# Kernel tuning notes

Hardware: AMD Instinct MI355X
Metric: run time of the kernel (lower is better)

Reference implementation:

```python
import jax, jax.numpy as jnp
import numpy as np

N_NODES = 32768
N_EDGES = 524288
EPS = 1e-5

def _layernorm(h):
    mu = jnp.mean(h, axis=-1, keepdims=True)
    var = jnp.var(h, axis=-1, keepdims=True)
    return (h - mu) / jnp.sqrt(var + EPS)

def _leaky_relu(h):
    return jnp.where(h >= 0, h, 0.01 * h)

def setup_inputs() -> dict:
    key = jax.random.key(0)
    ks = jax.random.split(key, 16)
    F, H, D = 256, 256, 1024
    x = jax.random.normal(ks[0], (N_NODES, F), dtype=jnp.float32)
    src = jax.random.randint(ks[1], (N_EDGES,), 0, N_NODES, dtype=jnp.int32)
    dst = jax.random.randint(ks[2], (N_EDGES,), 0, N_NODES, dtype=jnp.int32)
    dims = [F, H, H, H, D]
    params = {}
    for i in range(4):
        params[f"W{i+1}"] = jax.random.normal(ks[3 + i], (dims[i], dims[i + 1]), dtype=jnp.float32) * (1.0 / np.sqrt(dims[i]))
        params[f"b{i+1}"] = jnp.zeros((dims[i + 1],), dtype=jnp.float32)
    Wm = jax.random.normal(ks[8], (D, D), dtype=jnp.float32) * (1.0 / np.sqrt(D))
    bm = jnp.zeros((D,), dtype=jnp.float32)
    Ws = jax.random.normal(ks[9], (D, D), dtype=jnp.float32) * (1.0 / np.sqrt(D))
    bs = jnp.zeros((D,), dtype=jnp.float32)
    return dict(x=x, src=src, dst=dst, W1=params["W1"], b1=params["b1"], W2=params["W2"], b2=params["b2"], W3=params["W3"], b3=params["b3"], W4=params["W4"], b4=params["b4"], Wm=Wm, bm=bm, Ws=Ws, bs=bs, batch_b=128, nodes_per=256)

def reference(x, src, dst, W1, b1, W2, b2, W3, b3, W4, b4, Wm, bm, Ws, bs, batch_b, nodes_per):
    # DGL GraphConv norm='both': out = D_in^{-1/2} * A @ (D_out^{-1/2} * h) @ W + b
    ones = jnp.ones((src.shape[0],), dtype=x.dtype)
    out_deg = jax.ops.segment_sum(ones, src, num_segments=N_NODES)
    in_deg = jax.ops.segment_sum(ones, dst, num_segments=N_NODES)
    ns = jnp.where(out_deg > 0, jax.lax.rsqrt(out_deg), 1.0)[:, None]
    nd = jnp.where(in_deg > 0, jax.lax.rsqrt(in_deg), 1.0)[:, None]

    def gconv(h, W, b):
        if W.shape[0] <= W.shape[1]:  # aggregate first, then project (in <= out)
            m = (h * ns)[src]
            agg = jax.ops.segment_sum(m, dst, num_segments=N_NODES) * nd
            return agg @ W + b
        else:  # project first
            h = (h * ns) @ W
            agg = jax.ops.segment_sum(h[src], dst, num_segments=N_NODES) * nd
            return agg + b

    h = x
    for (W, b) in [(W1, b1), (W2, b2), (W3, b3), (W4, b4)]:
        h = _layernorm(_leaky_relu(gconv(h, W, b)))
    h = h.reshape(batch_b, nodes_per, -1)  # [B, N_per, D]
    h = jnp.mean(h, axis=1)                # AvePool over nodes
    h = _layernorm(h)
    mean = h @ Wm + bm
    log_std = h @ Ws + bs
    return (mean, log_std)
```

## Files before the change

### kernel.cpp

```cpp
#include <hip/hip_runtime.h>

#define N_NODES 32768
#define N_EDGES 524288

typedef __attribute__((ext_vector_type(8))) short short8;
typedef __attribute__((ext_vector_type(4))) float floatx4;

#define GLOBAL_AS __attribute__((address_space(1)))
#define LDS_AS __attribute__((address_space(3)))

__device__ __forceinline__ unsigned short f2bf(float x) {
    union { float f; unsigned u; } v; v.f = x;
    unsigned r = v.u + 0x7FFF + ((v.u >> 16) & 1);
    return (unsigned short)(r >> 16);
}
__device__ __forceinline__ float bf2f(unsigned short u) {
    union { unsigned u; float f; } v; v.u = ((unsigned)u) << 16;
    return v.f;
}


__global__ __launch_bounds__(256) void k_hist(const int* __restrict__ src,
                                              const int* __restrict__ dst,
                                              unsigned int* __restrict__ histOut32,
                                              unsigned int* __restrict__ histIn32) {
    __shared__ unsigned int hOut[8192];
    __shared__ unsigned int hIn[8192];
    int t = threadIdx.x, b = blockIdx.x;
    for (int i = t; i < 8192; i += 256) { hOut[i] = 0; hIn[i] = 0; }
    __syncthreads();
    int base = b * 4096;
    for (int i = t; i < 4096; i += 256) {
        int s = src[base + i], d = dst[base + i];
        atomicAdd(&hOut[s >> 2], 1u << ((s & 3) * 8));
        atomicAdd(&hIn[d >> 2], 1u << ((d & 3) * 8));
    }
    __syncthreads();
    for (int i = t; i < 8192; i += 256) {
        histOut32[b * 8192 + i] = hOut[i];
        histIn32[b * 8192 + i] = hIn[i];
    }
}

__global__ __launch_bounds__(256) void k_merge(const unsigned int* __restrict__ histOut32,
                                               const unsigned int* __restrict__ histIn32,
                                               unsigned int* __restrict__ pre32,
                                               int* __restrict__ in_deg,
                                               float* __restrict__ ns,
                                               float* __restrict__ nd) {
    int g = blockIdx.x * 256 + threadIdx.x;
    int ri0 = 0, ri1 = 0, ri2 = 0, ri3 = 0;
    for (int b = 0; b < 128; b++) {
        pre32[b * 8192 + g] = (unsigned)ri0 | ((unsigned)ri1 << 8) |
                              ((unsigned)ri2 << 16) | ((unsigned)ri3 << 24);
        unsigned int v = histIn32[b * 8192 + g];
        ri0 += v & 255; ri1 += (v >> 8) & 255; ri2 += (v >> 16) & 255; ri3 += (v >> 24) & 255;
    }
    in_deg[g * 4 + 0] = ri0; in_deg[g * 4 + 1] = ri1;
    in_deg[g * 4 + 2] = ri2; in_deg[g * 4 + 3] = ri3;
    nd[g * 4 + 0] = ri0 > 0 ? rsqrtf((float)ri0) : 1.0f;
    nd[g * 4 + 1] = ri1 > 0 ? rsqrtf((float)ri1) : 1.0f;
    nd[g * 4 + 2] = ri2 > 0 ? rsqrtf((float)ri2) : 1.0f;
    nd[g * 4 + 3] = ri3 > 0 ? rsqrtf((float)ri3) : 1.0f;
    int ro0 = 0, ro1 = 0, ro2 = 0, ro3 = 0;
    for (int b = 0; b < 128; b++) {
        unsigned int v = histOut32[b * 8192 + g];
        ro0 += v & 255; ro1 += (v >> 8) & 255; ro2 += (v >> 16) & 255; ro3 += (v >> 24) & 255;
    }
    ns[g * 4 + 0] = ro0 > 0 ? rsqrtf((float)ro0) : 1.0f;
    ns[g * 4 + 1] = ro1 > 0 ? rsqrtf((float)ro1) : 1.0f;
    ns[g * 4 + 2] = ro2 > 0 ? rsqrtf((float)ro2) : 1.0f;
    ns[g * 4 + 3] = ro3 > 0 ? rsqrtf((float)ro3) : 1.0f;
}

__global__ void k_scan(const int* __restrict__ in_deg, int* __restrict__ row_ptr) {
    __shared__ int part[1024];
    int t = threadIdx.x;
    int base = t * 32;
    int local[32];
    int s = 0;
    for (int i = 0; i < 32; i++) { local[i] = s; s += in_deg[base + i]; }
    part[t] = s;
    __syncthreads();
    for (int off = 1; off < 1024; off <<= 1) {
        int v = (t >= off) ? part[t - off] : 0;
        __syncthreads();
        part[t] += v;
        __syncthreads();
    }
    int prev = (t == 0) ? 0 : part[t - 1];
    for (int i = 0; i < 32; i++) row_ptr[base + i] = prev + local[i];
    if (t == 1023) row_ptr[N_NODES] = part[1023];
}

__global__ __launch_bounds__(256) void k_place(const int* __restrict__ src,
                                               const int* __restrict__ dst,
                                               const unsigned int* __restrict__ pre32,
                                               const int* __restrict__ row_ptr,
                                               int* __restrict__ csr_src) {
    __shared__ unsigned int cur[8192];
    int t = threadIdx.x, b = blockIdx.x;
    for (int i = t; i < 8192; i += 256) cur[i] = 0;
    __syncthreads();
    int base = b * 4096;
    const unsigned int* preb = pre32 + b * 8192;
    for (int i = t; i < 4096; i += 256) {
        int s = src[base + i], d = dst[base + i];
        int sh = (d & 3) * 8;
        unsigned int old = atomicAdd(&cur[d >> 2], 1u << sh);
        int rank = (old >> sh) & 255;
        int pb = (preb[d >> 2] >> sh) & 255;
        csr_src[row_ptr[d] + pb + rank] = s;
    }
}

struct TransDescs {
    const float* W[6];
    unsigned short* Wt[6];
    int K[6], N[6];
    int end[6];
};

__global__ __launch_bounds__(256) void k_transpose_all(TransDescs d) {
    int id = blockIdx.x, s = 0;
#pragma unroll
    for (int i = 0; i < 6; i++) if (id >= d.end[i]) s = i + 1;
    int base = (s == 0) ? 0 : d.end[s - 1];
    int t = id - base;
    int K = d.K[s], N = d.N[s];
    int ncols = N >> 5;
    int n0 = (t % ncols) * 32, k0 = (t / ncols) * 32;
    const float* W = d.W[s];
    unsigned short* Wt = d.Wt[s];
    __shared__ float tile[32][33];
    int tx = threadIdx.x & 31, ty = threadIdx.x >> 5;
    for (int r = 0; r < 32; r += 8)
        tile[ty + r][tx] = W[(size_t)(k0 + ty + r) * N + n0 + tx];
    __syncthreads();
    for (int r = 0; r < 32; r += 8)
        Wt[(size_t)(n0 + ty + r) * K + k0 + tx] = f2bf(tile[tx][ty + r]);
}

__global__ __launch_bounds__(256) void k_scale_x(const float* __restrict__ x,
                                                 const float* __restrict__ ns,
                                                 unsigned short* __restrict__ xsb) {
    int i = blockIdx.x * 256 + threadIdx.x;
    float4 v = ((const float4*)x)[i];
    int n = i >> 6;
    int f = (i & 63) * 4;
    float sc = ns[n];
    ushort4 o;
    o.x = f2bf(v.x * sc); o.y = f2bf(v.y * sc);
    o.z = f2bf(v.z * sc); o.w = f2bf(v.w * sc);
    size_t off = (size_t)(f >> 6) * (N_NODES * 64) + (size_t)n * 64 + (f & 63);
    *(ushort4*)(xsb + off) = o;
}

__global__ __launch_bounds__(512, 4) void fused_layer(
        const unsigned short* __restrict__ hs,
        const int* __restrict__ row_ptr,
        const int* __restrict__ csr_src,
        const float* __restrict__ nd,
        const unsigned short* __restrict__ Bt,
        const float* __restrict__ bias,
        const float* __restrict__ ns,
        unsigned short* __restrict__ ho) {
    __shared__ __align__(16) unsigned short At[8 * 2048];
    __shared__ __align__(16) unsigned short Bs[2][256 * 32];
    __shared__ int eIdx[2048];
    __shared__ int rp[65];
    __shared__ float sSum[4][64], sSum2[4][64], sMa[64], sMb[64];
    const int tid = threadIdx.x;
    const int lane = tid & 63;
    const int w = tid >> 6;
    const int n0 = blockIdx.x * 64;
    const int K = 256;

    const int pr = lane >> 3;
    const int uu = (lane & 7) ^ pr;
    const int rowInGrp = pr * 2 + (uu >> 2);
    const int kc = (uu & 3) * 8;
    const unsigned short* gB = Bt + (size_t)(w * 32 + rowInGrp) * K + kc;
    const int bBase = (w * 32) * 32;
#define STAGEB(buf_, koff_)                                                              \
    {                                                                                    \
        unsigned short* lB = Bs[buf_] + bBase;                                           \
        __builtin_amdgcn_global_load_lds((const GLOBAL_AS short*)(gB + (koff_)),         \
                                         (LDS_AS short*)lB, 16, 0, 0);                   \
        __builtin_amdgcn_global_load_lds((const GLOBAL_AS short*)(gB + (koff_) + (size_t)16 * K), \
                                         (LDS_AS short*)(lB + 16 * 32), 16, 0, 0);       \
    }
    STAGEB(0, 0)

    if (tid <= 64) rp[tid] = row_ptr[n0 + tid];
    __syncthreads();
    const int ebeg = rp[0];
    const int ecount = rp[64] - ebeg;
    const int ecached = ecount < 2048 ? ecount : 2048;
    for (int i = tid; i < ecached; i += 512) eIdx[i] = csr_src[ebeg + i];
    __syncthreads();

    const int r = tid >> 3;
    const int fs = tid & 7;
    const int beg = rp[r] - ebeg, end = rp[r + 1] - ebeg;
    const float sc = nd[n0 + r];
    const int rowpair = r >> 1;
    unsigned short* atp = At + rowpair * 64 +
                          (((((r & 1) << 2) | (fs & 3)) ^ (rowpair & 7)) << 3);

    auto sweep = [&](auto fetch) {
        for (int c = 0; c < 4; c++) {
            const unsigned short* hp = hs + (size_t)c * (N_NODES * 64) + fs * 8;
            float acc[8];
#pragma unroll
            for (int k = 0; k < 8; k++) acc[k] = 0.f;
            int e = beg;
            for (; e + 8 <= end; e += 8) {
                int s0 = fetch(e),     s1 = fetch(e + 1), s2 = fetch(e + 2), s3 = fetch(e + 3);
                int s4 = fetch(e + 4), s5 = fetch(e + 5), s6 = fetch(e + 6), s7 = fetch(e + 7);
                short8 v0 = *(const short8*)(hp + (size_t)s0 * 64);
                short8 v1 = *(const short8*)(hp + (size_t)s1 * 64);
                short8 v2 = *(const short8*)(hp + (size_t)s2 * 64);
                short8 v3 = *(const short8*)(hp + (size_t)s3 * 64);
                short8 v4 = *(const short8*)(hp + (size_t)s4 * 64);
                short8 v5 = *(const short8*)(hp + (size_t)s5 * 64);
                short8 v6 = *(const short8*)(hp + (size_t)s6 * 64);
                short8 v7 = *(const short8*)(hp + (size_t)s7 * 64);
#pragma unroll
                for (int k = 0; k < 8; k++)
                    acc[k] += ((bf2f((unsigned short)v0[k]) + bf2f((unsigned short)v1[k])) +
                               (bf2f((unsigned short)v2[k]) + bf2f((unsigned short)v3[k]))) +
                              ((bf2f((unsigned short)v4[k]) + bf2f((unsigned short)v5[k])) +
                               (bf2f((unsigned short)v6[k]) + bf2f((unsigned short)v7[k])));
            }
            for (; e + 2 <= end; e += 2) {
                int s0 = fetch(e), s1 = fetch(e + 1);
                short8 v0 = *(const short8*)(hp + (size_t)s0 * 64);
                short8 v1 = *(const short8*)(hp + (size_t)s1 * 64);
#pragma unroll
                for (int k = 0; k < 8; k++)
                    acc[k] += bf2f((unsigned short)v0[k]) + bf2f((unsigned short)v1[k]);
            }
            if (e < end) {
                int s = fetch(e);
                short8 v = *(const short8*)(hp + (size_t)s * 64);
#pragma unroll
                for (int k = 0; k < 8; k++) acc[k] += bf2f((unsigned short)v[k]);
            }
            short8 o;
#pragma unroll
            for (int k = 0; k < 8; k++) o[k] = (short)f2bf(acc[k] * sc);
            *(short8*)(atp + (c * 2 + (fs >> 2)) * 2048) = o;
        }
    };
    if (ecount <= 2048)
        sweep([&](int e) { return eIdx[e]; });
    else
        sweep([&](int e) { return csr_src[ebeg + e]; });

    const int wr = (w >> 2) * 32;
    const int wc = (w & 3) * 64;
    floatx4 acc2[2][4];
#pragma unroll
    for (int i = 0; i < 2; i++)
#pragma unroll
        for (int j = 0; j < 4; j++) acc2[i][j] = (floatx4){0.f, 0.f, 0.f, 0.f};
    const int q = lane >> 4;
    const int ln = lane & 15;
    const int uf = (((ln & 1) << 2) | q) ^ ((ln >> 1) & 7);

    int buf = 0;
    for (int k0 = 0; k0 < K; k0 += 32) {
        __syncthreads();
        if (k0 + 32 < K) STAGEB(buf ^ 1, k0 + 32)
        const unsigned short* rA = At + (k0 >> 5) * 2048;
        const unsigned short* rB = Bs[buf];
        short8 af[2], bfr[4];
#pragma unroll
        for (int i = 0; i < 2; i++)
            af[i] = *(const short8*)(rA + (((wr + i * 16 + ln) >> 1) << 6) + uf * 8);
#pragma unroll
        for (int j = 0; j < 4; j++)
            bfr[j] = *(const short8*)(rB + (((wc + j * 16 + ln) >> 1) << 6) + uf * 8);
#pragma unroll
        for (int i = 0; i < 2; i++)
#pragma unroll
            for (int j = 0; j < 4; j++)
                acc2[i][j] = __builtin_amdgcn_mfma_f32_16x16x32_bf16(af[i], bfr[j], acc2[i][j], 0, 0, 0);
        buf ^= 1;
    }
#undef STAGEB

    float bcol[4];
#pragma unroll
    for (int j = 0; j < 4; j++) bcol[j] = bias[wc + j * 16 + ln];
    const int wcIdx = w & 3;
#pragma unroll
    for (int i = 0; i < 2; i++) {
#pragma unroll
        for (int rr = 0; rr < 4; rr++) {
            float s = 0.f, s2 = 0.f;
#pragma unroll
            for (int j = 0; j < 4; j++) {
                float v = acc2[i][j][rr] + bcol[j];
                v = v >= 0.f ? v : 0.01f * v;
                s += v; s2 += v * v;
            }
#pragma unroll
            for (int off = 8; off > 0; off >>= 1) {
                s += __shfl_down(s, off, 16);
                s2 += __shfl_down(s2, off, 16);
            }
            if (ln == 0) {
                int row = wr + i * 16 + q * 4 + rr;
                sSum[wcIdx][row] = s;
                sSum2[wcIdx][row] = s2;
            }
        }
    }
    __syncthreads();
    if (tid < 64) {
        float su = sSum[0][tid] + sSum[1][tid] + sSum[2][tid] + sSum[3][tid];
        float su2 = sSum2[0][tid] + sSum2[1][tid] + sSum2[2][tid] + sSum2[3][tid];
        float mu = su * (1.0f / 256.0f);
        float var = su2 * (1.0f / 256.0f) - mu * mu;
        float rs = rsqrtf(var + 1e-5f);
        float nsv = ns[n0 + tid];
        sMa[tid] = rs * nsv;
        sMb[tid] = -mu * rs * nsv;
    }
    __syncthreads();
#pragma unroll
    for (int i = 0; i < 2; i++) {
#pragma unroll
        for (int rr = 0; rr < 4; rr++) {
            int row = wr + i * 16 + q * 4 + rr;
            float a = sMa[row], bb = sMb[row];
#pragma unroll
            for (int j = 0; j < 4; j++) {
                float v = acc2[i][j][rr] + bcol[j];
                v = v >= 0.f ? v : 0.01f * v;
                int col = wc + j * 16 + ln;
                size_t off = (size_t)(col >> 6) * (N_NODES * 64) +
                             (size_t)(n0 + row) * 64 + (col & 63);
                ho[off] = f2bf(v * a + bb);
            }
        }
    }
}

__global__ __launch_bounds__(128, 8) void k_aggregate(
        const unsigned short* __restrict__ hs,
        const int* __restrict__ row_ptr,
        const int* __restrict__ csr_src,
        const float* __restrict__ nd,
        unsigned short* __restrict__ aggb) {
    __shared__ int eIdx[512];
    __shared__ int rp[17];
    const int tid = threadIdx.x;
    const int n0 = blockIdx.x * 16;
    if (tid <= 16) rp[tid] = row_ptr[n0 + tid];
    __syncthreads();
    const int ebeg = rp[0];
    const int ecount = rp[16] - ebeg;
    const int ecached = ecount < 512 ? ecount : 512;
    for (int i = tid; i < ecached; i += 128) eIdx[i] = csr_src[ebeg + i];
    __syncthreads();

    const int nl = tid >> 3;
    const int fs = tid & 7;
    const int n = n0 + nl;
    const int beg = rp[nl] - ebeg, end = rp[nl + 1] - ebeg;
    const float sc = nd[n];

    auto sweep = [&](auto fetch) {
        for (int c = 0; c < 4; c++) {
            const unsigned short* hp = hs + (size_t)c * (N_NODES * 64) + fs * 8;
            float acc[8];
#pragma unroll
            for (int k = 0; k < 8; k++) acc[k] = 0.f;
            int e = beg;
            for (; e + 8 <= end; e += 8) {
                int s0 = fetch(e),     s1 = fetch(e + 1), s2 = fetch(e + 2), s3 = fetch(e + 3);
                int s4 = fetch(e + 4), s5 = fetch(e + 5), s6 = fetch(e + 6), s7 = fetch(e + 7);
                short8 v0 = *(const short8*)(hp + (size_t)s0 * 64);
                short8 v1 = *(const short8*)(hp + (size_t)s1 * 64);
                short8 v2 = *(const short8*)(hp + (size_t)s2 * 64);
                short8 v3 = *(const short8*)(hp + (size_t)s3 * 64);
                short8 v4 = *(const short8*)(hp + (size_t)s4 * 64);
                short8 v5 = *(const short8*)(hp + (size_t)s5 * 64);
                short8 v6 = *(const short8*)(hp + (size_t)s6 * 64);
                short8 v7 = *(const short8*)(hp + (size_t)s7 * 64);
#pragma unroll
                for (int k = 0; k < 8; k++)
                    acc[k] += ((bf2f((unsigned short)v0[k]) + bf2f((unsigned short)v1[k])) +
                               (bf2f((unsigned short)v2[k]) + bf2f((unsigned short)v3[k]))) +
                              ((bf2f((unsigned short)v4[k]) + bf2f((unsigned short)v5[k])) +
                               (bf2f((unsigned short)v6[k]) + bf2f((unsigned short)v7[k])));
            }
            for (; e + 2 <= end; e += 2) {
                int s0 = fetch(e), s1 = fetch(e + 1);
                short8 v0 = *(const short8*)(hp + (size_t)s0 * 64);
                short8 v1 = *(const short8*)(hp + (size_t)s1 * 64);
#pragma unroll
                for (int k = 0; k < 8; k++)
                    acc[k] += bf2f((unsigned short)v0[k]) + bf2f((unsigned short)v1[k]);
            }
            if (e < end) {
                int s = fetch(e);
                short8 v = *(const short8*)(hp + (size_t)s * 64);
#pragma unroll
                for (int k = 0; k < 8; k++) acc[k] += bf2f((unsigned short)v[k]);
            }
            short8 o;
#pragma unroll
            for (int k = 0; k < 8; k++) o[k] = (short)f2bf(acc[k] * sc);
            __builtin_nontemporal_store(o, (short8*)(aggb + (size_t)n * 256 + c * 64 + fs * 8));
        }
    };
    if (ecount <= 512)
        sweep([&](int e) { return eIdx[e]; });
    else
        sweep([&](int e) { return csr_src[ebeg + e]; });
}

template <bool LEAKY, bool OUT_BF16>
__global__ __launch_bounds__(256) void gemm_mfma(
        const unsigned short* __restrict__ A, const unsigned short* __restrict__ Bt,
        const float* __restrict__ bias,
        void* __restrict__ Cv,
        int M, int N, int K) {
    __shared__ __align__(16) unsigned short As[2][128 * 32];
    __shared__ __align__(16) unsigned short Bs[2][128 * 32];
    const int tid = threadIdx.x;
    const int lane = tid & 63;
    const int w = tid >> 6;
    const int wr = (w >> 1) * 64;
    const int wc = (w & 1) * 64;
    const int rowBase = blockIdx.x * 128;
    const int colBase = blockIdx.y * 128;

    floatx4 acc[4][4];
#pragma unroll
    for (int i = 0; i < 4; i++)
#pragma unroll
        for (int j = 0; j < 4; j++) acc[i][j] = (floatx4){0.f, 0.f, 0.f, 0.f};

    const int pr = lane >> 3;
    const int uu = (lane & 7) ^ pr;
    const int srow = w * 32 + pr * 2 + (uu >> 2);
    const int kc = (uu & 3) * 8;
    const unsigned short* gA = A + (size_t)(rowBase + srow) * K + kc;
    const unsigned short* gB = Bt + (size_t)(colBase + srow) * K + kc;
    const int wbase = (w * 32) * 32;

    const int q = lane >> 4;
    const int ln = lane & 15;
    const int uf = (((ln & 1) << 2) | q) ^ ((ln >> 1) & 7);

    {
        unsigned short* lA = As[0] + wbase;
        unsigned short* lB = Bs[0] + wbase;
        __builtin_amdgcn_global_load_lds((const GLOBAL_AS short*)(gA),
                                         (LDS_AS short*)lA, 16, 0, 0);
        __builtin_amdgcn_global_load_lds((const GLOBAL_AS short*)(gA + (size_t)16 * K),
                                         (LDS_AS short*)(lA + 16 * 32), 16, 0, 0);
        __builtin_amdgcn_global_load_lds((const GLOBAL_AS short*)(gB),
                                         (LDS_AS short*)lB, 16, 0, 0);
        __builtin_amdgcn_global_load_lds((const GLOBAL_AS short*)(gB + (size_t)16 * K),
                                         (LDS_AS short*)(lB + 16 * 32), 16, 0, 0);
    }

    int buf = 0;
    for (int k0 = 0; k0 < K; k0 += 32) {
        __syncthreads();
        if (k0 + 32 < K) {
            unsigned short* lA = As[buf ^ 1] + wbase;
            unsigned short* lB = Bs[buf ^ 1] + wbase;
            __builtin_amdgcn_global_load_lds((const GLOBAL_AS short*)(gA + k0 + 32),
                                             (LDS_AS short*)lA, 16, 0, 0);
            __builtin_amdgcn_global_load_lds((const GLOBAL_AS short*)(gA + k0 + 32 + (size_t)16 * K),
                                             (LDS_AS short*)(lA + 16 * 32), 16, 0, 0);
            __builtin_amdgcn_global_load_lds((const GLOBAL_AS short*)(gB + k0 + 32),
                                             (LDS_AS short*)lB, 16, 0, 0);
            __builtin_amdgcn_global_load_lds((const GLOBAL_AS short*)(gB + k0 + 32 + (size_t)16 * K),
                                             (LDS_AS short*)(lB + 16 * 32), 16, 0, 0);
        }
        const unsigned short* rA = As[buf];
        const unsigned short* rB = Bs[buf];
        short8 af[4], bfr[4];
#pragma unroll
        for (int i = 0; i < 4; i++)
            af[i] = *(const short8*)(rA + (((wr + i * 16 + ln) >> 1) << 6) + uf * 8);
#pragma unroll
        for (int j = 0; j < 4; j++)
            bfr[j] = *(const short8*)(rB + (((wc + j * 16 + ln) >> 1) << 6) + uf * 8);
#pragma unroll
        for (int i = 0; i < 4; i++)
#pragma unroll
            for (int j = 0; j < 4; j++)
                acc[i][j] = __builtin_amdgcn_mfma_f32_16x16x32_bf16(af[i], bfr[j], acc[i][j], 0, 0, 0);
        buf ^= 1;
    }
#pragma unroll
    for (int i = 0; i < 4; i++) {
#pragma unroll
        for (int j = 0; j < 4; j++) {
#pragma unroll
            for (int r = 0; r < 4; r++) {
                int row = rowBase + wr + i * 16 + q * 4 + r;
                int col = colBase + wc + j * 16 + ln;
                float v = acc[i][j][r] + bias[col];
                if (LEAKY) v = v >= 0.f ? v : 0.01f * v;
                if (OUT_BF16)
                    ((unsigned short*)Cv)[(size_t)row * N + col] = f2bf(v);
                else
                    ((float*)Cv)[(size_t)row * N + col] = v;
            }
        }
    }
}

__global__ __launch_bounds__(256) void gemm_heads(
        const unsigned short* __restrict__ A,
        const unsigned short* __restrict__ Bt,
        float* __restrict__ P) {
    __shared__ __align__(16) unsigned short As[2][128 * 32];
    __shared__ __align__(16) unsigned short Bs[2][128 * 32];
    const int tid = threadIdx.x;
    const int lane = tid & 63;
    const int w = tid >> 6;
    const int wr = (w >> 1) * 64;
    const int wc = (w & 1) * 64;
    const int colBase = blockIdx.x * 128;
    const int ks = blockIdx.y;
    const int K = 1024;

    floatx4 acc[4][4];
#pragma unroll
    for (int i = 0; i < 4; i++)
#pragma unroll
        for (int j = 0; j < 4; j++) acc[i][j] = (floatx4){0.f, 0.f, 0.f, 0.f};

    const int pr = lane >> 3;
    const int uu = (lane & 7) ^ pr;
    const int srow = w * 32 + pr * 2 + (uu >> 2);
    const int kc = (uu & 3) * 8;
    const unsigned short* gA = A + (size_t)srow * K + ks * 128 + kc;
    const unsigned short* gB = Bt + (size_t)(colBase + srow) * K + ks * 128 + kc;
    const int wbase = (w * 32) * 32;

    const int q = lane >> 4;
    const int ln = lane & 15;
    const int uf = (((ln & 1) << 2) | q) ^ ((ln >> 1) & 7);

    {
        unsigned short* lA = As[0] + wbase;
        unsigned short* lB = Bs[0] + wbase;
        __builtin_amdgcn_global_load_lds((const GLOBAL_AS short*)(gA),
                                         (LDS_AS short*)lA, 16, 0, 0);
        __builtin_amdgcn_global_load_lds((const GLOBAL_AS short*)(gA + (size_t)16 * K),
                                         (LDS_AS short*)(lA + 16 * 32), 16, 0, 0);
        __builtin_amdgcn_global_load_lds((const GLOBAL_AS short*)(gB),
                                         (LDS_AS short*)lB, 16, 0, 0);
        __builtin_amdgcn_global_load_lds((const GLOBAL_AS short*)(gB + (size_t)16 * K),
                                         (LDS_AS short*)(lB + 16 * 32), 16, 0, 0);
    }

    int buf = 0;
    for (int k0 = 0; k0 < 128; k0 += 32) {
        __syncthreads();
        if (k0 + 32 < 128) {
            unsigned short* lA = As[buf ^ 1] + wbase;
            unsigned short* lB = Bs[buf ^ 1] + wbase;
            __builtin_amdgcn_global_load_lds((const GLOBAL_AS short*)(gA + k0 + 32),
                                             (LDS_AS short*)lA, 16, 0, 0);
            __builtin_amdgcn_global_load_lds((const GLOBAL_AS short*)(gA + k0 + 32 + (size_t)16 * K),
                                             (LDS_AS short*)(lA + 16 * 32), 16, 0, 0);
            __builtin_amdgcn_global_load_lds((const GLOBAL_AS short*)(gB + k0 + 32),
                                             (LDS_AS short*)lB, 16, 0, 0);
            __builtin_amdgcn_global_load_lds((const GLOBAL_AS short*)(gB + k0 + 32 + (size_t)16 * K),
                                             (LDS_AS short*)(lB + 16 * 32), 16, 0, 0);
        }
        const unsigned short* rA = As[buf];
        const unsigned short* rB = Bs[buf];
        short8 af[4], bfr[4];
#pragma unroll
        for (int i = 0; i < 4; i++)
            af[i] = *(const short8*)(rA + (((wr + i * 16 + ln) >> 1) << 6) + uf * 8);
#pragma unroll
        for (int j = 0; j < 4; j++)
            bfr[j] = *(const short8*)(rB + (((wc + j * 16 + ln) >> 1) << 6) + uf * 8);
#pragma unroll
        for (int i = 0; i < 4; i++)
#pragma unroll
            for (int j = 0; j < 4; j++)
                acc[i][j] = __builtin_amdgcn_mfma_f32_16x16x32_bf16(af[i], bfr[j], acc[i][j], 0, 0, 0);
        buf ^= 1;
    }
    float* Pk = P + (size_t)ks * 128 * 2048;
#pragma unroll
    for (int i = 0; i < 4; i++) {
#pragma unroll
        for (int j = 0; j < 4; j++) {
#pragma unroll
            for (int r = 0; r < 4; r++) {
                int row = wr + i * 16 + q * 4 + r;
                int col = colBase + wc + j * 16 + ln;
                Pk[(size_t)row * 2048 + col] = acc[i][j][r];
            }
        }
    }
}

__global__ __launch_bounds__(256) void k_heads_reduce(
        const float* __restrict__ P, const float* __restrict__ bm,
        const float* __restrict__ bsd, float* __restrict__ out) {
    int idx = blockIdx.x * 256 + threadIdx.x;
    int row = idx >> 9;
    int col = (idx & 511) * 4;
    floatx4 s = (floatx4){0.f, 0.f, 0.f, 0.f};
#pragma unroll
    for (int p = 0; p < 8; p++)
        s += *(const floatx4*)(P + (size_t)p * 128 * 2048 + (size_t)row * 2048 + col);
    bool hi = col >= 1024;
    const float* bias = hi ? bsd : bm;
    int bc = hi ? col - 1024 : col;
    s += *(const floatx4*)(bias + bc);
    float* o = hi ? (out + (size_t)128 * 1024 + (size_t)row * 1024 + bc)
                  : (out + (size_t)row * 1024 + col);
    *(floatx4*)o = s;
}

__global__ __launch_bounds__(256) void k_lnpool(const unsigned short* __restrict__ h4,
                                                float* __restrict__ partial) {
    const int g = blockIdx.y, p = blockIdx.x;
    const int w = threadIdx.x >> 6, lane = threadIdx.x & 63;
    float acc[16];
#pragma unroll
    for (int k = 0; k < 16; k++) acc[k] = 0.f;
    for (int i = 0; i < 8; i++) {
        int node = (g * 8 + p) * 32 + w * 8 + i;
        const unsigned short* row = h4 + (size_t)node * 1024 + lane * 16;
        short8 a = *(const short8*)row;
        short8 b = *(const short8*)(row + 8);
        float v[16];
#pragma unroll
        for (int k = 0; k < 8; k++) v[k] = bf2f((unsigned short)a[k]);
#pragma unroll
        for (int k = 0; k < 8; k++) v[8 + k] = bf2f((unsigned short)b[k]);
        float s = 0.f, s2 = 0.f;
#pragma unroll
        for (int k = 0; k < 16; k++) { s += v[k]; s2 += v[k] * v[k]; }
#pragma unroll
        for (int off = 32; off > 0; off >>= 1) {
            s += __shfl_down(s, off);
            s2 += __shfl_down(s2, off);
        }
        s = __shfl(s, 0);
        s2 = __shfl(s2, 0);
        float mu = s * (1.0f / 1024.0f);
        float var = s2 * (1.0f / 1024.0f) - mu * mu;
        float rs = rsqrtf(var + 1e-5f);
#pragma unroll
        for (int k = 0; k < 16; k++) acc[k] += (v[k] - mu) * rs;
    }
    __shared__ float red[4][1024];
    float* my = red[w] + lane * 16;
#pragma unroll
    for (int k = 0; k < 16; k++) my[k] = acc[k];
    __syncthreads();
    int t = threadIdx.x;
    floatx4 o = (floatx4){0.f, 0.f, 0.f, 0.f};
#pragma unroll
    for (int w2 = 0; w2 < 4; w2++) {
        const floatx4 v = *(const floatx4*)(red[w2] + t * 4);
        o += v;
    }
    __builtin_nontemporal_store(o, (floatx4*)(partial + (size_t)(g * 8 + p) * 1024 + t * 4));
}

__global__ __launch_bounds__(256) void k_pool_final(const float* __restrict__ partial,
                                                    unsigned short* __restrict__ pooledb) {
    int g = blockIdx.x, t = threadIdx.x;
    int wave = t >> 6;
    float4 a = make_float4(0.f, 0.f, 0.f, 0.f);
    for (int p = 0; p < 8; p++) {
        float4 v = *(const float4*)(partial + (size_t)(g * 8 + p) * 1024 + t * 4);
        a.x += v.x; a.y += v.y; a.z += v.z; a.w += v.w;
    }
    const float invn = 1.0f / 256.0f;
    a.x *= invn; a.y *= invn; a.z *= invn; a.w *= invn;
    float s = a.x + a.y + a.z + a.w;
    float s2 = a.x * a.x + a.y * a.y + a.z * a.z + a.w * a.w;
#pragma unroll
    for (int off = 32; off > 0; off >>= 1) {
        s += __shfl_down(s, off);
        s2 += __shfl_down(s2, off);
    }
    __shared__ float ss[4], ss2[4];
    if ((t & 63) == 0) { ss[wave] = s; ss2[wave] = s2; }
    __syncthreads();
    if (t == 0) {
        float tt = 0.f, tt2 = 0.f;
        for (int w = 0; w < 4; w++) { tt += ss[w]; tt2 += ss2[w]; }
        float mu = tt / 1024.f;
        float var = tt2 / 1024.f - mu * mu;
        ss[0] = mu;
        ss2[0] = rsqrtf(var + 1e-5f);
    }
    __syncthreads();
    float mu = ss[0], inv = ss2[0];
    ushort4 o;
    o.x = f2bf((a.x - mu) * inv); o.y = f2bf((a.y - mu) * inv);
    o.z = f2bf((a.z - mu) * inv); o.w = f2bf((a.w - mu) * inv);
    *(ushort4*)(pooledb + (size_t)g * 1024 + t * 4) = o;
}

extern "C" void kernel_launch(void* const* d_in, const int* in_sizes, int n_in,
                              void* d_out, int out_size, void* d_ws, size_t ws_size,
                              hipStream_t stream) {
    const float* x  = (const float*)d_in[0];
    const int*   src = (const int*)d_in[1];
    const int*   dst = (const int*)d_in[2];
    const float* W1 = (const float*)d_in[3];  const float* b1 = (const float*)d_in[4];
    const float* W2 = (const float*)d_in[5];  const float* b2 = (const float*)d_in[6];
    const float* W3 = (const float*)d_in[7];  const float* b3 = (const float*)d_in[8];
    const float* W4 = (const float*)d_in[9];  const float* b4 = (const float*)d_in[10];
    const float* Wm = (const float*)d_in[11]; const float* bm = (const float*)d_in[12];
    const float* Wsd = (const float*)d_in[13]; const float* bsd = (const float*)d_in[14];
    float* out = (float*)d_out;

    char* w = (char*)d_ws;
    unsigned short* aggb = (unsigned short*)w; w += (size_t)N_NODES * 256 * 2;
    unsigned short* hsbA = (unsigned short*)w; w += (size_t)N_NODES * 256 * 2;
    unsigned short* hsbB = (unsigned short*)w; w += (size_t)N_NODES * 256 * 2;
    unsigned short* h4b  = (unsigned short*)w; w += (size_t)N_NODES * 1024 * 2;
    float* partial = (float*)w; w += (size_t)128 * 8 * 1024 * 4;
    unsigned short* pooledb = (unsigned short*)w; w += (size_t)128 * 1024 * 2;
    unsigned short* W1t = (unsigned short*)w; w += (size_t)256 * 256 * 2;
    unsigned short* W2t = (unsigned short*)w; w += (size_t)256 * 256 * 2;
    unsigned short* W3t = (unsigned short*)w; w += (size_t)256 * 256 * 2;
    unsigned short* W4t = (unsigned short*)w; w += (size_t)256 * 1024 * 2;
    unsigned short* Wmt = (unsigned short*)w; w += (size_t)1024 * 1024 * 2;
    unsigned short* Wst = (unsigned short*)w; w += (size_t)1024 * 1024 * 2;
    float* ns     = (float*)w; w += (size_t)N_NODES * 4;
    float* nd     = (float*)w; w += (size_t)N_NODES * 4;
    unsigned int* histOut32 = (unsigned int*)w; w += (size_t)128 * 8192 * 4;
    unsigned int* histIn32  = (unsigned int*)w; w += (size_t)128 * 8192 * 4;
    unsigned int* pre32     = (unsigned int*)w; w += (size_t)128 * 8192 * 4;
    int* in_deg   = (int*)w;   w += (size_t)N_NODES * 4;
    int* row_ptr  = (int*)w;   w += (size_t)(N_NODES + 1) * 4;
    int* csr_src  = (int*)w;   w += (size_t)N_EDGES * 4;
    float* headp = (float*)histOut32;

    TransDescs td;
    td.W[0] = W1; td.W[1] = W2; td.W[2] = W3; td.W[3] = W4; td.W[4] = Wm; td.W[5] = Wsd;
    td.Wt[0] = W1t; td.Wt[1] = W2t; td.Wt[2] = W3t; td.Wt[3] = W4t; td.Wt[4] = Wmt; td.Wt[5] = Wst;
    td.K[0] = 256; td.K[1] = 256; td.K[2] = 256; td.K[3] = 256; td.K[4] = 1024; td.K[5] = 1024;
    td.N[0] = 256; td.N[1] = 256; td.N[2] = 256; td.N[3] = 1024; td.N[4] = 1024; td.N[5] = 1024;
    td.end[0] = 64; td.end[1] = 128; td.end[2] = 192; td.end[3] = 448; td.end[4] = 1472; td.end[5] = 2496;
    k_transpose_all<<<2496, 256, 0, stream>>>(td);

    k_hist<<<128, 256, 0, stream>>>(src, dst, histOut32, histIn32);
    k_merge<<<32, 256, 0, stream>>>(histOut32, histIn32, pre32, in_deg, ns, nd);
    k_scan<<<1, 1024, 0, stream>>>(in_deg, row_ptr);
    k_place<<<128, 256, 0, stream>>>(src, dst, pre32, row_ptr, csr_src);

    k_scale_x<<<N_NODES * 256 / 1024, 256, 0, stream>>>(x, ns, hsbA);

    const unsigned short* Wts[3] = {W1t, W2t, W3t};
    const float* bs3[3] = {b1, b2, b3};
    unsigned short* tin = hsbA;
    unsigned short* tout = hsbB;
    for (int l = 0; l < 3; l++) {
        fused_layer<<<N_NODES / 64, 512, 0, stream>>>(tin, row_ptr, csr_src, nd,
                                                      Wts[l], bs3[l], ns, tout);
        unsigned short* tmp = tin; tin = tout; tout = tmp;
    }

    k_aggregate<<<N_NODES / 16, 128, 0, stream>>>(tin, row_ptr, csr_src, nd, aggb);
    gemm_mfma<true, true><<<dim3(N_NODES / 128, 8), 256, 0, stream>>>(
        aggb, W4t, b4, h4b, N_NODES, 1024, 256);

    k_lnpool<<<dim3(8, 128), 256, 0, stream>>>(h4b, partial);
    k_pool_final<<<128, 256, 0, stream>>>(partial, pooledb);

    gemm_heads<<<dim3(16, 8), 256, 0, stream>>>(pooledb, Wmt, headp);
    k_heads_reduce<<<256, 256, 0, stream>>>(headp, bm, bsd, out);
}
```

Measured before the change: 363.5 us.

## Fuse layer-4 aggregation with GEMM and parallelize degree merge and scan

```diff
diff --git a/kernel.cpp b/kernel.cpp
--- a/kernel.cpp
+++ b/kernel.cpp
@@ -42,55 +42,96 @@
     }
 }
 
-__global__ __launch_bounds__(256) void k_merge(const unsigned int* __restrict__ histOut32,
-                                               const unsigned int* __restrict__ histIn32,
-                                               unsigned int* __restrict__ pre32,
-                                               int* __restrict__ in_deg,
-                                               float* __restrict__ ns,
-                                               float* __restrict__ nd) {
+__global__ __launch_bounds__(256) void k_merge_p1(const unsigned int* __restrict__ histIn32,
+                                                  const unsigned int* __restrict__ histOut32,
+                                                  unsigned int* __restrict__ partIn,
+                                                  unsigned int* __restrict__ partOut) {
     int g = blockIdx.x * 256 + threadIdx.x;
-    int ri0 = 0, ri1 = 0, ri2 = 0, ri3 = 0;
-    for (int b = 0; b < 128; b++) {
-        pre32[b * 8192 + g] = (unsigned)ri0 | ((unsigned)ri1 << 8) |
-                              ((unsigned)ri2 << 16) | ((unsigned)ri3 << 24);
-        unsigned int v = histIn32[b * 8192 + g];
-        ri0 += v & 255; ri1 += (v >> 8) & 255; ri2 += (v >> 16) & 255; ri3 += (v >> 24) & 255;
-    }
-    in_deg[g * 4 + 0] = ri0; in_deg[g * 4 + 1] = ri1;
-    in_deg[g * 4 + 2] = ri2; in_deg[g * 4 + 3] = ri3;
-    nd[g * 4 + 0] = ri0 > 0 ? rsqrtf((float)ri0) : 1.0f;
-    nd[g * 4 + 1] = ri1 > 0 ? rsqrtf((float)ri1) : 1.0f;
-    nd[g * 4 + 2] = ri2 > 0 ? rsqrtf((float)ri2) : 1.0f;
-    nd[g * 4 + 3] = ri3 > 0 ? rsqrtf((float)ri3) : 1.0f;
-    int ro0 = 0, ro1 = 0, ro2 = 0, ro3 = 0;
-    for (int b = 0; b < 128; b++) {
-        unsigned int v = histOut32[b * 8192 + g];
-        ro0 += v & 255; ro1 += (v >> 8) & 255; ro2 += (v >> 16) & 255; ro3 += (v >> 24) & 255;
-    }
-    ns[g * 4 + 0] = ro0 > 0 ? rsqrtf((float)ro0) : 1.0f;
-    ns[g * 4 + 1] = ro1 > 0 ? rsqrtf((float)ro1) : 1.0f;
-    ns[g * 4 + 2] = ro2 > 0 ? rsqrtf((float)ro2) : 1.0f;
-    ns[g * 4 + 3] = ro3 > 0 ? rsqrtf((float)ro3) : 1.0f;
-}
-
-__global__ void k_scan(const int* __restrict__ in_deg, int* __restrict__ row_ptr) {
-    __shared__ int part[1024];
-    int t = threadIdx.x;
-    int base = t * 32;
-    int local[32];
-    int s = 0;
-    for (int i = 0; i < 32; i++) { local[i] = s; s += in_deg[base + i]; }
-    part[t] = s;
-    __syncthreads();
-    for (int off = 1; off < 1024; off <<= 1) {
+    int bg = blockIdx.y;
+    unsigned int si = 0, so = 0;
+#pragma unroll
+    for (int j = 0; j < 16; j++) {
+        si += histIn32[(bg * 16 + j) * 8192 + g];
+        so += histOut32[(bg * 16 + j) * 8192 + g];
+    }
+    partIn[bg * 8192 + g] = si;
+    partOut[bg * 8192 + g] = so;
+}
+
+__global__ __launch_bounds__(256) void k_merge_p2(const unsigned int* __restrict__ histIn32,
+                                                  const unsigned int* __restrict__ partIn,
+                                                  const unsigned int* __restrict__ partOut,
+                                                  unsigned int* __restrict__ pre32,
+                                                  int* __restrict__ in_deg,
+                                                  float* __restrict__ ns,
+                                                  float* __restrict__ nd) {
+    int g = blockIdx.x * 256 + threadIdx.x;
+    int bg = blockIdx.y;
+    unsigned int run = 0;
+    for (int b2 = 0; b2 < bg; b2++) run += partIn[b2 * 8192 + g];
+    for (int j = 0; j < 16; j++) {
+        int b = bg * 16 + j;
+        pre32[b * 8192 + g] = run;
+        run += histIn32[b * 8192 + g];
+    }
+    if (bg == 7) {
+        int r0 = run & 255, r1 = (run >> 8) & 255, r2 = (run >> 16) & 255, r3 = (run >> 24) & 255;
+        in_deg[g * 4 + 0] = r0; in_deg[g * 4 + 1] = r1;
+        in_deg[g * 4 + 2] = r2; in_deg[g * 4 + 3] = r3;
+        nd[g * 4 + 0] = r0 > 0 ? rsqrtf((float)r0) : 1.0f;
+        nd[g * 4 + 1] = r1 > 0 ? rsqrtf((float)r1) : 1.0f;
+        nd[g * 4 + 2] = r2 > 0 ? rsqrtf((float)r2) : 1.0f;
+        nd[g * 4 + 3] = r3 > 0 ? rsqrtf((float)r3) : 1.0f;
+    }
+    if (bg == 0) {
+        unsigned int to = 0;
+#pragma unroll
+        for (int b2 = 0; b2 < 8; b2++) to += partOut[b2 * 8192 + g];
+        int r0 = to & 255, r1 = (to >> 8) & 255, r2 = (to >> 16) & 255, r3 = (to >> 24) & 255;
+        ns[g * 4 + 0] = r0 > 0 ? rsqrtf((float)r0) : 1.0f;
+        ns[g * 4 + 1] = r1 > 0 ? rsqrtf((float)r1) : 1.0f;
+        ns[g * 4 + 2] = r2 > 0 ? rsqrtf((float)r2) : 1.0f;
+        ns[g * 4 + 3] = r3 > 0 ? rsqrtf((float)r3) : 1.0f;
+    }
+}
+
+__global__ __launch_bounds__(256) void k_scanA(const int* __restrict__ in_deg,
+                                               int* __restrict__ row_ptr,
+                                               int* __restrict__ blkSum) {
+    __shared__ int part[256];
+    int t = threadIdx.x, b = blockIdx.x;
+    int base = (b * 256 + t) * 4;
+    int l0 = in_deg[base], l1 = in_deg[base + 1], l2 = in_deg[base + 2], l3 = in_deg[base + 3];
+    part[t] = l0 + l1 + l2 + l3;
+    __syncthreads();
+    for (int off = 1; off < 256; off <<= 1) {
         int v = (t >= off) ? part[t - off] : 0;
         __syncthreads();
         part[t] += v;
         __syncthreads();
     }
-    int prev = (t == 0) ? 0 : part[t - 1];
-    for (int i = 0; i < 32; i++) row_ptr[base + i] = prev + local[i];
-    if (t == 1023) row_ptr[N_NODES] = part[1023];
+    int excl = (t == 0) ? 0 : part[t - 1];
+    row_ptr[base] = excl;
+    row_ptr[base + 1] = excl + l0;
+    row_ptr[base + 2] = excl + l0 + l1;
+    row_ptr[base + 3] = excl + l0 + l1 + l2;
+    if (t == 255) blkSum[b] = part[255];
+}
+
+__global__ __launch_bounds__(256) void k_scanC(const int* __restrict__ blkSum,
+                                               int* __restrict__ row_ptr) {
+    __shared__ int soff;
+    int t = threadIdx.x, b = blockIdx.x;
+    if (t == 0) {
+        int s = 0;
+        for (int i = 0; i < b; i++) s += blkSum[i];
+        soff = s;
+    }
+    __syncthreads();
+    int base = (b * 256 + t) * 4;
+    row_ptr[base] += soff; row_ptr[base + 1] += soff;
+    row_ptr[base + 2] += soff; row_ptr[base + 3] += soff;
+    if (b == 31 && t == 255) row_ptr[N_NODES] = soff + blkSum[31];
 }
 
 __global__ __launch_bounds__(256) void k_place(const int* __restrict__ src,
@@ -349,29 +390,55 @@
     }
 }
 
-__global__ __launch_bounds__(128, 8) void k_aggregate(
+__global__ __launch_bounds__(512, 4) void fused_layer4(
         const unsigned short* __restrict__ hs,
         const int* __restrict__ row_ptr,
         const int* __restrict__ csr_src,
         const float* __restrict__ nd,
-        unsigned short* __restrict__ aggb) {
-    __shared__ int eIdx[512];
-    __shared__ int rp[17];
+        const unsigned short* __restrict__ Bt,
+        const float* __restrict__ bias,
+        unsigned short* __restrict__ h4) {
+    __shared__ __align__(16) unsigned short At[8 * 2048];
+    __shared__ __align__(16) unsigned short Bs[2][256 * 32];
+    __shared__ int eIdx[2048];
+    __shared__ int rp[65];
     const int tid = threadIdx.x;
-    const int n0 = blockIdx.x * 16;
-    if (tid <= 16) rp[tid] = row_ptr[n0 + tid];
+    const int lane = tid & 63;
+    const int w = tid >> 6;
+    const int n0 = blockIdx.x * 64;
+    const int K = 256;
+
+    const int pr = lane >> 3;
+    const int uu = (lane & 7) ^ pr;
+    const int rowInGrp = pr * 2 + (uu >> 2);
+    const int kc = (uu & 3) * 8;
+    const int bBase = (w * 32) * 32;
+#define STAGEB4(buf_, ct_, koff_)                                                        \
+    {                                                                                    \
+        const unsigned short* gB = Bt + (size_t)((ct_) * 256 + w * 32 + rowInGrp) * K + kc; \
+        unsigned short* lB = Bs[buf_] + bBase;                                           \
+        __builtin_amdgcn_global_load_lds((const GLOBAL_AS short*)(gB + (koff_)),         \
+                                         (LDS_AS short*)lB, 16, 0, 0);                   \
+        __builtin_amdgcn_global_load_lds((const GLOBAL_AS short*)(gB + (koff_) + (size_t)16 * K), \
+                                         (LDS_AS short*)(lB + 16 * 32), 16, 0, 0);       \
+    }
+    STAGEB4(0, 0, 0)
+
+    if (tid <= 64) rp[tid] = row_ptr[n0 + tid];
     __syncthreads();
     const int ebeg = rp[0];
-    const int ecount = rp[16] - ebeg;
-    const int ecached = ecount < 512 ? ecount : 512;
-    for (int i = tid; i < ecached; i += 128) eIdx[i] = csr_src[ebeg + i];
-    __syncthreads();
-
-    const int nl = tid >> 3;
+    const int ecount = rp[64] - ebeg;
+    const int ecached = ecount < 2048 ? ecount : 2048;
+    for (int i = tid; i < ecached; i += 512) eIdx[i] = csr_src[ebeg + i];
+    __syncthreads();
+
+    const int r = tid >> 3;
     const int fs = tid & 7;
-    const int n = n0 + nl;
-    const int beg = rp[nl] - ebeg, end = rp[nl + 1] - ebeg;
-    const float sc = nd[n];
+    const int beg = rp[r] - ebeg, end = rp[r + 1] - ebeg;
+    const float sc = nd[n0 + r];
+    const int rowpair = r >> 1;
+    unsigned short* atp = At + rowpair * 64 +
+                          (((((r & 1) << 2) | (fs & 3)) ^ (rowpair & 7)) << 3);
 
     auto sweep = [&](auto fetch) {
         for (int c = 0; c < 4; c++) {
@@ -415,110 +482,66 @@
             short8 o;
 #pragma unroll
             for (int k = 0; k < 8; k++) o[k] = (short)f2bf(acc[k] * sc);
-            __builtin_nontemporal_store(o, (short8*)(aggb + (size_t)n * 256 + c * 64 + fs * 8));
+            *(short8*)(atp + (c * 2 + (fs >> 2)) * 2048) = o;
         }
     };
-    if (ecount <= 512)
+    if (ecount <= 2048)
         sweep([&](int e) { return eIdx[e]; });
     else
         sweep([&](int e) { return csr_src[ebeg + e]; });
-}
-
-template <bool LEAKY, bool OUT_BF16>
-__global__ __launch_bounds__(256) void gemm_mfma(
-        const unsigned short* __restrict__ A, const unsigned short* __restrict__ Bt,
-        const float* __restrict__ bias,
-        void* __restrict__ Cv,
-        int M, int N, int K) {
-    __shared__ __align__(16) unsigned short As[2][128 * 32];
-    __shared__ __align__(16) unsigned short Bs[2][128 * 32];
-    const int tid = threadIdx.x;
-    const int lane = tid & 63;
-    const int w = tid >> 6;
-    const int wr = (w >> 1) * 64;
-    const int wc = (w & 1) * 64;
-    const int rowBase = blockIdx.x * 128;
-    const int colBase = blockIdx.y * 128;
-
-    floatx4 acc[4][4];
-#pragma unroll
-    for (int i = 0; i < 4; i++)
-#pragma unroll
-        for (int j = 0; j < 4; j++) acc[i][j] = (floatx4){0.f, 0.f, 0.f, 0.f};
-
-    const int pr = lane >> 3;
-    const int uu = (lane & 7) ^ pr;
-    const int srow = w * 32 + pr * 2 + (uu >> 2);
-    const int kc = (uu & 3) * 8;
-    const unsigned short* gA = A + (size_t)(rowBase + srow) * K + kc;
-    const unsigned short* gB = Bt + (size_t)(colBase + srow) * K + kc;
-    const int wbase = (w * 32) * 32;
-
+
+    const int wr = (w >> 2) * 32;
+    const int wc = (w & 3) * 64;
     const int q = lane >> 4;
     const int ln = lane & 15;
     const int uf = (((ln & 1) << 2) | q) ^ ((ln >> 1) & 7);
 
-    {
-        unsigned short* lA = As[0] + wbase;
-        unsigned short* lB = Bs[0] + wbase;
-        __builtin_amdgcn_global_load_lds((const GLOBAL_AS short*)(gA),
-                                         (LDS_AS short*)lA, 16, 0, 0);
-        __builtin_amdgcn_global_load_lds((const GLOBAL_AS short*)(gA + (size_t)16 * K),
-                                         (LDS_AS short*)(lA + 16 * 32), 16, 0, 0);
-        __builtin_amdgcn_global_load_lds((const GLOBAL_AS short*)(gB),
-                                         (LDS_AS short*)lB, 16, 0, 0);
-        __builtin_amdgcn_global_load_lds((const GLOBAL_AS short*)(gB + (size_t)16 * K),
-                                         (LDS_AS short*)(lB + 16 * 32), 16, 0, 0);
-    }
-
     int buf = 0;
-    for (int k0 = 0; k0 < K; k0 += 32) {
-        __syncthreads();
-        if (k0 + 32 < K) {
-            unsigned short* lA = As[buf ^ 1] + wbase;
-            unsigned short* lB = Bs[buf ^ 1] + wbase;
-            __builtin_amdgcn_global_load_lds((const GLOBAL_AS short*)(gA + k0 + 32),
-                                             (LDS_AS short*)lA, 16, 0, 0);
-            __builtin_amdgcn_global_load_lds((const GLOBAL_AS short*)(gA + k0 + 32 + (size_t)16 * K),
-                                             (LDS_AS short*)(lA + 16 * 32), 16, 0, 0);
-            __builtin_amdgcn_global_load_lds((const GLOBAL_AS short*)(gB + k0 + 32),
-                                             (LDS_AS short*)lB, 16, 0, 0);
-            __builtin_amdgcn_global_load_lds((const GLOBAL_AS short*)(gB + k0 + 32 + (size_t)16 * K),
-                                             (LDS_AS short*)(lB + 16 * 32), 16, 0, 0);
+    for (int ct = 0; ct < 4; ct++) {
+        floatx4 acc2[2][4];
+#pragma unroll
+        for (int i = 0; i < 2; i++)
+#pragma unroll
+            for (int j = 0; j < 4; j++) acc2[i][j] = (floatx4){0.f, 0.f, 0.f, 0.f};
+        for (int k0 = 0; k0 < K; k0 += 32) {
+            __syncthreads();
+            if (k0 + 32 < K) {
+                STAGEB4(buf ^ 1, ct, k0 + 32)
+            } else if (ct < 3) {
+                STAGEB4(buf ^ 1, ct + 1, 0)
+            }
+            const unsigned short* rA = At + (k0 >> 5) * 2048;
+            const unsigned short* rB = Bs[buf];
+            short8 af[2], bfr[4];
+#pragma unroll
+            for (int i = 0; i < 2; i++)
+                af[i] = *(const short8*)(rA + (((wr + i * 16 + ln) >> 1) << 6) + uf * 8);
+#pragma unroll
+            for (int j = 0; j < 4; j++)
+                bfr[j] = *(const short8*)(rB + (((wc + j * 16 + ln) >> 1) << 6) + uf * 8);
+#pragma unroll
+            for (int i = 0; i < 2; i++)
+#pragma unroll
+                for (int j = 0; j < 4; j++)
+                    acc2[i][j] = __builtin_amdgcn_mfma_f32_16x16x32_bf16(af[i], bfr[j], acc2[i][j], 0, 0, 0);
+            buf ^= 1;
         }
-        const unsigned short* rA = As[buf];
-        const unsigned short* rB = Bs[buf];
-        short8 af[4], bfr[4];
-#pragma unroll
-        for (int i = 0; i < 4; i++)
-            af[i] = *(const short8*)(rA + (((wr + i * 16 + ln) >> 1) << 6) + uf * 8);
-#pragma unroll
-        for (int j = 0; j < 4; j++)
-            bfr[j] = *(const short8*)(rB + (((wc + j * 16 + ln) >> 1) << 6) + uf * 8);
-#pragma unroll
-        for (int i = 0; i < 4; i++)
-#pragma unroll
-            for (int j = 0; j < 4; j++)
-                acc[i][j] = __builtin_amdgcn_mfma_f32_16x16x32_bf16(af[i], bfr[j], acc[i][j], 0, 0, 0);
-        buf ^= 1;
-    }
-#pragma unroll
-    for (int i = 0; i < 4; i++) {
-#pragma unroll
-        for (int j = 0; j < 4; j++) {
-#pragma unroll
-            for (int r = 0; r < 4; r++) {
-                int row = rowBase + wr + i * 16 + q * 4 + r;
-                int col = colBase + wc + j * 16 + ln;
-                float v = acc[i][j][r] + bias[col];
-                if (LEAKY) v = v >= 0.f ? v : 0.01f * v;
-                if (OUT_BF16)
-                    ((unsigned short*)Cv)[(size_t)row * N + col] = f2bf(v);
-                else
-                    ((float*)Cv)[(size_t)row * N + col] = v;
+#pragma unroll
+        for (int i = 0; i < 2; i++) {
+#pragma unroll
+            for (int rr = 0; rr < 4; rr++) {
+                int row = wr + i * 16 + q * 4 + rr;
+#pragma unroll
+                for (int j = 0; j < 4; j++) {
+                    int col = ct * 256 + wc + j * 16 + ln;
+                    float v = acc2[i][j][rr] + bias[col];
+                    v = v >= 0.f ? v : 0.01f * v;
+                    h4[(size_t)(n0 + row) * 1024 + col] = f2bf(v);
+                }
             }
         }
     }
+#undef STAGEB4
 }
 
 __global__ __launch_bounds__(256) void gemm_heads(
@@ -732,7 +755,6 @@
     float* out = (float*)d_out;
 
     char* w = (char*)d_ws;
-    unsigned short* aggb = (unsigned short*)w; w += (size_t)N_NODES * 256 * 2;
     unsigned short* hsbA = (unsigned short*)w; w += (size_t)N_NODES * 256 * 2;
     unsigned short* hsbB = (unsigned short*)w; w += (size_t)N_NODES * 256 * 2;
     unsigned short* h4b  = (unsigned short*)w; w += (size_t)N_NODES * 1024 * 2;
@@ -749,6 +771,9 @@
     unsigned int* histOut32 = (unsigned int*)w; w += (size_t)128 * 8192 * 4;
     unsigned int* histIn32  = (unsigned int*)w; w += (size_t)128 * 8192 * 4;
     unsigned int* pre32     = (unsigned int*)w; w += (size_t)128 * 8192 * 4;
+    unsigned int* partIn    = (unsigned int*)w; w += (size_t)8 * 8192 * 4;
+    unsigned int* partOut   = (unsigned int*)w; w += (size_t)8 * 8192 * 4;
+    int* blkSum   = (int*)w;   w += (size_t)64 * 4;
     int* in_deg   = (int*)w;   w += (size_t)N_NODES * 4;
     int* row_ptr  = (int*)w;   w += (size_t)(N_NODES + 1) * 4;
     int* csr_src  = (int*)w;   w += (size_t)N_EDGES * 4;
@@ -763,8 +788,10 @@
     k_transpose_all<<<2496, 256, 0, stream>>>(td);
 
     k_hist<<<128, 256, 0, stream>>>(src, dst, histOut32, histIn32);
-    k_merge<<<32, 256, 0, stream>>>(histOut32, histIn32, pre32, in_deg, ns, nd);
-    k_scan<<<1, 1024, 0, stream>>>(in_deg, row_ptr);
+    k_merge_p1<<<dim3(32, 8), 256, 0, stream>>>(histIn32, histOut32, partIn, partOut);
+    k_merge_p2<<<dim3(32, 8), 256, 0, stream>>>(histIn32, partIn, partOut, pre32, in_deg, ns, nd);
+    k_scanA<<<32, 256, 0, stream>>>(in_deg, row_ptr, blkSum);
+    k_scanC<<<32, 256, 0, stream>>>(blkSum, row_ptr);
     k_place<<<128, 256, 0, stream>>>(src, dst, pre32, row_ptr, csr_src);
 
     k_scale_x<<<N_NODES * 256 / 1024, 256, 0, stream>>>(x, ns, hsbA);
@@ -779,9 +806,8 @@
         unsigned short* tmp = tin; tin = tout; tout = tmp;
     }
 
-    k_aggregate<<<N_NODES / 16, 128, 0, stream>>>(tin, row_ptr, csr_src, nd, aggb);
-    gemm_mfma<true, true><<<dim3(N_NODES / 128, 8), 256, 0, stream>>>(
-        aggb, W4t, b4, h4b, N_NODES, 1024, 256);
+    fused_layer4<<<N_NODES / 64, 512, 0, stream>>>(tin, row_ptr, csr_src, nd,
+                                                   W4t, b4, h4b);
 
     k_lnpool<<<dim3(8, 128), 256, 0, stream>>>(h4b, partial);
     k_pool_final<<<128, 256, 0, stream>>>(partial, pooledb);
```

Measured after the change: 336.3 us, median of 2. 7.5% less time.
